# Performance work log

Measured on AMD Instinct MI355X. Metric: run time of the kernel, lower is better.

The kernel has to match this reference:

```python
import jax, jax.numpy as jnp
import numpy as np

B, N, KNB, F, H = 1, 50000, 16, 128, 128
BN_EPS = 1e-3  # keras BatchNormalization default epsilon
ALPHA = 0.3    # keras LeakyReLU default negative slope


def setup_inputs() -> dict:
    key = jax.random.key(0)
    ks = jax.random.split(key, 14)
    s_in = 1.0 / np.sqrt(F)
    s_cat = 1.0 / np.sqrt(F + H)
    return {
        'embeddings': jax.random.normal(ks[0], (B, N, F), jnp.float32),
        'weights': jnp.zeros((1, 1), jnp.float32),  # unused in call_att
        'neighbor_set': jax.random.randint(ks[1], (B, N, KNB), 0, N),
        'Wq': jax.random.normal(ks[2], (F, H), jnp.float32) * s_in,
        'bq': jnp.zeros((H,), jnp.float32),
        'Wk': jax.random.normal(ks[3], (F, H), jnp.float32) * s_in,
        'bk': jnp.zeros((H,), jnp.float32),
        'Wv': jax.random.normal(ks[4], (F, H), jnp.float32) * s_in,
        'bv': jnp.zeros((H,), jnp.float32),
        'W1': jax.random.normal(ks[5], (F + H, H), jnp.float32) * s_cat,
        'b1': jnp.zeros((H,), jnp.float32),
        'gamma': 1.0 + 0.1 * jax.random.normal(ks[6], (H,), jnp.float32),
        'beta': 0.1 * jax.random.normal(ks[7], (H,), jnp.float32),
        'mov_mean': 0.1 * jax.random.normal(ks[8], (H,), jnp.float32),
        'mov_var': 1.0 + 0.1 * jax.random.uniform(ks[9], (H,), jnp.float32),
    }


def reference(embeddings, weights, neighbor_set, Wq, bq, Wk, bk, Wv, bv,
              W1, b1, gamma, beta, mov_mean, mov_var):
    lrelu = lambda x: jax.nn.leaky_relu(x, ALPHA)
    # batched gather: nb[b, n, k] = embeddings[b, neighbor_set[b, n, k]]  -> [B,N,K,F]
    nb = jax.vmap(lambda e, idx: e[idx])(embeddings, neighbor_set)
    q = lrelu(embeddings @ Wq + bq)      # [B,N,H]
    k = lrelu(nb @ Wk + bk)              # [B,N,K,H]
    v = lrelu(nb @ Wv + bv)              # [B,N,K,H]
    # Q is tiled across the K neighbor rows in the original; every attention row
    # is identical, so mean-pool over rows == single-query attention. Same math.
    scores = jnp.einsum('bnh,bnkh->bnk', q, k)          # dot-product, no scale
    attn = jax.nn.softmax(scores, axis=-1)
    pooled = jnp.einsum('bnk,bnkh->bnh', attn, v)       # [B,N,H]
    h = lrelu(jnp.concatenate([embeddings, pooled], axis=-1) @ W1 + b1)
    h = h / (jnp.linalg.norm(h, axis=2, keepdims=True) + 1e-6)
    # BatchNormalization (inference form, axis=-1)
    return gamma * (h - mov_mean) * jax.lax.rsqrt(mov_var + BN_EPS) + beta
```

## Files before the change

### kernel.cpp

```cpp
#include <hip/hip_runtime.h>
#include <hip/hip_bf16.h>

#define N_NODES 50000
#define KNB 16
#define FDIM 128
#define HDIM 128
#define ALPHA 0.3f
#define BN_EPS 1e-3f

typedef __bf16 v8bf __attribute__((ext_vector_type(8)));
typedef float v4f __attribute__((ext_vector_type(4)));
typedef unsigned short ushort_t;

__device__ __forceinline__ float blo(unsigned int u) {
    union { float f; unsigned int i; } x; x.i = u << 16; return x.f;
}
__device__ __forceinline__ float bhi(unsigned int u) {
    union { float f; unsigned int i; } x; x.i = u & 0xffff0000u; return x.f;
}

__device__ __forceinline__ unsigned short f2bf(float f) {
    union { float f; unsigned int u; } x;
    x.f = f;
    unsigned int r = x.u + 0x7fffu + ((x.u >> 16) & 1u);
    return (unsigned short)(r >> 16);
}

__device__ __forceinline__ unsigned int pk2(float a, float b) {
    __hip_bfloat162 h = __float22bfloat162_rn(make_float2(a, b));
    union { __hip_bfloat162 h; unsigned int u; } r; r.h = h; return r.u;
}

__device__ __forceinline__ float lrelu(float x) { return x > 0.f ? x : ALPHA * x; }

__device__ __forceinline__ v8bf load8f(const float* p) {
    float4 A = ((const float4*)p)[0];
    float4 B = ((const float4*)p)[1];
    union { v8bf v; unsigned int u[4]; } r;
    r.u[0] = pk2(A.x, A.y); r.u[1] = pk2(A.z, A.w);
    r.u[2] = pk2(B.x, B.y); r.u[3] = pk2(B.z, B.w);
    return r.v;
}

__global__ __launch_bounds__(256) void prep_kernel(
    const float* __restrict__ Wq, const float* __restrict__ Wk,
    const float* __restrict__ Wv, const float* __restrict__ W1,
    ushort_t* __restrict__ WT)
{
    const int idx = blockIdx.x * 256 + threadIdx.x;
    if (idx < 16384) {
        int k = idx >> 7, n = idx & 127;
        WT[n * 128 + k] = f2bf(Wq[idx]);
    } else if (idx < 32768) {
        int i = idx - 16384; int k = i >> 7, n = i & 127;
        WT[16384 + n * 128 + k] = f2bf(Wk[i]);
    } else if (idx < 49152) {
        int i = idx - 32768; int k = i >> 7, n = i & 127;
        WT[32768 + n * 128 + k] = f2bf(Wv[i]);
    } else if (idx < 81920) {
        int i = idx - 49152; int k = i >> 7, n = i & 127;
        WT[49152 + n * 256 + k] = f2bf(W1[i]);
    }
}

__global__ __launch_bounds__(256) void qkv_kernel(
    const float* __restrict__ E, const ushort_t* __restrict__ WT,
    const float* __restrict__ bq, const float* __restrict__ bk,
    const float* __restrict__ bv,
    float* __restrict__ Qo, ushort_t* __restrict__ KV)
{
    __shared__ ushort_t sW[128 * 136];

    const int tid  = threadIdx.x;
    const int wave = tid >> 6;
    const int lane = tid & 63;
    const int quad = lane >> 4;
    const int j    = lane & 15;
    const int row0 = blockIdx.x * 128 + wave * 32;

    const int ar0 = min(row0 + j,      N_NODES - 1);
    const int ar1 = min(row0 + 16 + j, N_NODES - 1);

    v8bf a0f[4], a1f[4];
#pragma unroll
    for (int ks = 0; ks < 4; ++ks) {
        const int k0 = ks * 32 + quad * 8;
        a0f[ks] = load8f(E + (size_t)ar0 * FDIM + k0);
        a1f[ks] = load8f(E + (size_t)ar1 * FDIM + k0);
    }

    const float* biases[3] = {bq, bk, bv};

    for (int w = 0; w < 3; ++w) {
        const ushort_t* Wsrc = WT + w * 16384;
        for (int i = tid; i < 2048; i += 256) {
            int n = i >> 4, kc = i & 15;
            *(uint4*)(&sW[n * 136 + kc * 8]) = *(const uint4*)(Wsrc + n * 128 + kc * 8);
        }
        __syncthreads();

        v4f acc[2][8];
#pragma unroll
        for (int rb = 0; rb < 2; ++rb)
#pragma unroll
            for (int c = 0; c < 8; ++c) acc[rb][c] = (v4f){0.f, 0.f, 0.f, 0.f};

#pragma unroll
        for (int ks = 0; ks < 4; ++ks) {
            const int k0 = ks * 32 + quad * 8;
            v8bf b[8];
#pragma unroll
            for (int c = 0; c < 8; ++c)
                b[c] = *(const v8bf*)(&sW[(c * 16 + j) * 136 + k0]);
#pragma unroll
            for (int c = 0; c < 8; ++c) {
                acc[0][c] = __builtin_amdgcn_mfma_f32_16x16x32_bf16(a0f[ks], b[c], acc[0][c], 0, 0, 0);
                acc[1][c] = __builtin_amdgcn_mfma_f32_16x16x32_bf16(a1f[ks], b[c], acc[1][c], 0, 0, 0);
            }
        }

        const float* bias = biases[w];
#pragma unroll
        for (int c = 0; c < 8; ++c) {
            const int col = c * 16 + j;
            const float bv_ = bias[col];
#pragma unroll
            for (int rb = 0; rb < 2; ++rb) {
#pragma unroll
                for (int i = 0; i < 4; ++i) {
                    const int r = row0 + rb * 16 + quad * 4 + i;
                    if (r < N_NODES) {
                        const float x = lrelu(acc[rb][c][i] + bv_);
                        if (w == 0)      Qo[(size_t)r * HDIM + col] = x;
                        else if (w == 1) KV[(size_t)r * 256 + col] = f2bf(x);
                        else             KV[(size_t)r * 256 + 128 + col] = f2bf(x);
                    }
                }
            }
        }
        __syncthreads();
    }
}

__global__ __launch_bounds__(256) void attn_kernel(
    float* __restrict__ QP, const ushort_t* __restrict__ KV,
    const int* __restrict__ nbr)
{
    const int tid  = threadIdx.x;
    const int wave = tid >> 6;
    const int lane = tid & 63;
    const int node = __builtin_amdgcn_readfirstlane(blockIdx.x * 4 + wave);

    const float2 qp = ((const float2*)(QP + (size_t)node * HDIM))[lane];

    int idxs[KNB];
    const int* nb = nbr + node * KNB;
#pragma unroll
    for (int t = 0; t < KNB; ++t) {
        int id = nb[t];
        idxs[t] = ((unsigned)id < (unsigned)N_NODES) ? id : 0;
    }

    float sc[KNB];
#pragma unroll
    for (int t = 0; t < KNB; ++t) {
        const unsigned int kp = ((const unsigned int*)(KV + (size_t)idxs[t] * 256))[lane];
        float p = qp.x * blo(kp) + qp.y * bhi(kp);
#pragma unroll
        for (int off = 32; off >= 1; off >>= 1) p += __shfl_xor(p, off, 64);
        sc[t] = p;
    }

    float m = sc[0];
#pragma unroll
    for (int t = 1; t < KNB; ++t) m = fmaxf(m, sc[t]);
    float s = 0.f;
#pragma unroll
    for (int t = 0; t < KNB; ++t) { sc[t] = __expf(sc[t] - m); s += sc[t]; }
    const float inv = 1.f / s;

    float p0 = 0.f, p1 = 0.f;
#pragma unroll
    for (int t = 0; t < KNB; ++t) {
        const unsigned int vp = ((const unsigned int*)(KV + (size_t)idxs[t] * 256 + 128))[lane];
        const float a = sc[t] * inv;
        p0 += a * blo(vp);
        p1 += a * bhi(vp);
    }

    ((float2*)(QP + (size_t)node * HDIM))[lane] = make_float2(p0, p1);
}

__global__ __launch_bounds__(256) void out_kernel(
    const float* __restrict__ E, const ushort_t* __restrict__ W1T,
    const float* __restrict__ b1,
    const float* __restrict__ gamma, const float* __restrict__ beta,
    const float* __restrict__ mmean, const float* __restrict__ mvar,
    float* __restrict__ OutP)
{
    __shared__ ushort_t sW[128 * 136];

    const int tid  = threadIdx.x;
    const int wave = tid >> 6;
    const int lane = tid & 63;
    const int quad = lane >> 4;
    const int j    = lane & 15;
    const int row0 = blockIdx.x * 128 + wave * 32;

    const int ar0 = min(row0 + j,      N_NODES - 1);
    const int ar1 = min(row0 + 16 + j, N_NODES - 1);

    v4f acc[2][8];
#pragma unroll
    for (int rb = 0; rb < 2; ++rb)
#pragma unroll
        for (int c = 0; c < 8; ++c) acc[rb][c] = (v4f){0.f, 0.f, 0.f, 0.f};

    for (int half = 0; half < 2; ++half) {
        for (int i = tid; i < 2048; i += 256) {
            int n = i >> 4, kc = i & 15;
            *(uint4*)(&sW[n * 136 + kc * 8]) =
                *(const uint4*)(W1T + n * 256 + half * 128 + kc * 8);
        }
        __syncthreads();

        const float* Abase = (half == 0) ? E : (const float*)OutP;
#pragma unroll
        for (int ks = 0; ks < 4; ++ks) {
            const int k0 = ks * 32 + quad * 8;
            v8bf a0 = load8f(Abase + (size_t)ar0 * 128 + k0);
            v8bf a1 = load8f(Abase + (size_t)ar1 * 128 + k0);
            v8bf b[8];
#pragma unroll
            for (int c = 0; c < 8; ++c)
                b[c] = *(const v8bf*)(&sW[(c * 16 + j) * 136 + k0]);
#pragma unroll
            for (int c = 0; c < 8; ++c) {
                acc[0][c] = __builtin_amdgcn_mfma_f32_16x16x32_bf16(a0, b[c], acc[0][c], 0, 0, 0);
                acc[1][c] = __builtin_amdgcn_mfma_f32_16x16x32_bf16(a1, b[c], acc[1][c], 0, 0, 0);
            }
        }
        __syncthreads();
    }

    float scale_[8], shift_[8], bias_[8];
#pragma unroll
    for (int c = 0; c < 8; ++c) {
        const int col = c * 16 + j;
        const float sc = gamma[col] * rsqrtf(mvar[col] + BN_EPS);
        scale_[c] = sc;
        shift_[c] = beta[col] - mmean[col] * sc;
        bias_[c]  = b1[col];
    }

#pragma unroll
    for (int rb = 0; rb < 2; ++rb)
#pragma unroll
        for (int c = 0; c < 8; ++c)
#pragma unroll
            for (int i = 0; i < 4; ++i)
                acc[rb][c][i] = lrelu(acc[rb][c][i] + bias_[c]);

#pragma unroll
    for (int rb = 0; rb < 2; ++rb) {
#pragma unroll
        for (int i = 0; i < 4; ++i) {
            float ss = 0.f;
#pragma unroll
            for (int c = 0; c < 8; ++c) ss += acc[rb][c][i] * acc[rb][c][i];
            ss += __shfl_xor(ss, 1, 64);
            ss += __shfl_xor(ss, 2, 64);
            ss += __shfl_xor(ss, 4, 64);
            ss += __shfl_xor(ss, 8, 64);
            const float invn = 1.f / (sqrtf(ss) + 1e-6f);
            const int r = row0 + rb * 16 + quad * 4 + i;
            if (r < N_NODES) {
#pragma unroll
                for (int c = 0; c < 8; ++c)
                    OutP[(size_t)r * HDIM + c * 16 + j] =
                        acc[rb][c][i] * invn * scale_[c] + shift_[c];
            }
        }
    }
}

extern "C" void kernel_launch(void* const* d_in, const int* in_sizes, int n_in,
                              void* d_out, int out_size, void* d_ws, size_t ws_size,
                              hipStream_t stream)
{
    const float* E     = (const float*)d_in[0];
    const int*   nbr   = (const int*)d_in[2];
    const float* Wq    = (const float*)d_in[3];
    const float* bq    = (const float*)d_in[4];
    const float* Wk    = (const float*)d_in[5];
    const float* bk    = (const float*)d_in[6];
    const float* Wv    = (const float*)d_in[7];
    const float* bv    = (const float*)d_in[8];
    const float* W1    = (const float*)d_in[9];
    const float* b1    = (const float*)d_in[10];
    const float* gam   = (const float*)d_in[11];
    const float* bet   = (const float*)d_in[12];
    const float* mmean = (const float*)d_in[13];
    const float* mvar  = (const float*)d_in[14];

    ushort_t* KV = (ushort_t*)d_ws;
    ushort_t* WT = KV + (size_t)N_NODES * 256;
    float* QP = (float*)d_out;

    const int gridA = (N_NODES + 127) / 128;
    prep_kernel<<<320, 256, 0, stream>>>(Wq, Wk, Wv, W1, WT);
    qkv_kernel<<<gridA, 256, 0, stream>>>(E, WT, bq, bk, bv, QP, KV);
    attn_kernel<<<N_NODES / 4, 256, 0, stream>>>(QP, KV, nbr);
    out_kernel<<<gridA, 256, 0, stream>>>(E, WT + 49152, b1, gam, bet, mmean, mvar, QP);
}
```

Measured before the change: 218.3 us.

## Split QKV projection across grid y and read weights directly from global

The QKV kernel now launches a 2D grid with one y-slice per projection (Q, K, V) instead of looping over the three weight matrices inside each block. Both the QKV and output kernels drop the shared-memory weight staging and its barriers, loading MFMA B fragments straight from global memory and relying on cache. This gives three times as many blocks and frees LDS for occupancy. The cost is that each embedding row is loaded three times and B-fragment loads become uncoalesced cached global reads instead of LDS reads.

```diff
diff --git a/kernel.cpp b/kernel.cpp
--- a/kernel.cpp
+++ b/kernel.cpp
@@ -69,14 +69,15 @@
     const float* __restrict__ bv,
     float* __restrict__ Qo, ushort_t* __restrict__ KV)
 {
-    __shared__ ushort_t sW[128 * 136];
-
     const int tid  = threadIdx.x;
     const int wave = tid >> 6;
     const int lane = tid & 63;
     const int quad = lane >> 4;
     const int j    = lane & 15;
     const int row0 = blockIdx.x * 128 + wave * 32;
+    const int w    = blockIdx.y;
+
+    const ushort_t* __restrict__ Wsrc = WT + w * 16384;
 
     const int ar0 = min(row0 + j,      N_NODES - 1);
     const int ar1 = min(row0 + 16 + j, N_NODES - 1);
@@ -89,56 +90,44 @@
         a1f[ks] = load8f(E + (size_t)ar1 * FDIM + k0);
     }
 
-    const float* biases[3] = {bq, bk, bv};
-
-    for (int w = 0; w < 3; ++w) {
-        const ushort_t* Wsrc = WT + w * 16384;
-        for (int i = tid; i < 2048; i += 256) {
-            int n = i >> 4, kc = i & 15;
-            *(uint4*)(&sW[n * 136 + kc * 8]) = *(const uint4*)(Wsrc + n * 128 + kc * 8);
-        }
-        __syncthreads();
-
-        v4f acc[2][8];
-#pragma unroll
-        for (int rb = 0; rb < 2; ++rb)
-#pragma unroll
-            for (int c = 0; c < 8; ++c) acc[rb][c] = (v4f){0.f, 0.f, 0.f, 0.f};
-
-#pragma unroll
-        for (int ks = 0; ks < 4; ++ks) {
-            const int k0 = ks * 32 + quad * 8;
-            v8bf b[8];
-#pragma unroll
-            for (int c = 0; c < 8; ++c)
-                b[c] = *(const v8bf*)(&sW[(c * 16 + j) * 136 + k0]);
-#pragma unroll
-            for (int c = 0; c < 8; ++c) {
-                acc[0][c] = __builtin_amdgcn_mfma_f32_16x16x32_bf16(a0f[ks], b[c], acc[0][c], 0, 0, 0);
-                acc[1][c] = __builtin_amdgcn_mfma_f32_16x16x32_bf16(a1f[ks], b[c], acc[1][c], 0, 0, 0);
-            }
-        }
-
-        const float* bias = biases[w];
+    v4f acc[2][8];
+#pragma unroll
+    for (int rb = 0; rb < 2; ++rb)
+#pragma unroll
+        for (int c = 0; c < 8; ++c) acc[rb][c] = (v4f){0.f, 0.f, 0.f, 0.f};
+
+#pragma unroll
+    for (int ks = 0; ks < 4; ++ks) {
+        const int k0 = ks * 32 + quad * 8;
+        v8bf b[8];
+#pragma unroll
+        for (int c = 0; c < 8; ++c)
+            b[c] = *(const v8bf*)(Wsrc + (c * 16 + j) * 128 + k0);
 #pragma unroll
         for (int c = 0; c < 8; ++c) {
-            const int col = c * 16 + j;
-            const float bv_ = bias[col];
-#pragma unroll
-            for (int rb = 0; rb < 2; ++rb) {
-#pragma unroll
-                for (int i = 0; i < 4; ++i) {
-                    const int r = row0 + rb * 16 + quad * 4 + i;
-                    if (r < N_NODES) {
-                        const float x = lrelu(acc[rb][c][i] + bv_);
-                        if (w == 0)      Qo[(size_t)r * HDIM + col] = x;
-                        else if (w == 1) KV[(size_t)r * 256 + col] = f2bf(x);
-                        else             KV[(size_t)r * 256 + 128 + col] = f2bf(x);
-                    }
+            acc[0][c] = __builtin_amdgcn_mfma_f32_16x16x32_bf16(a0f[ks], b[c], acc[0][c], 0, 0, 0);
+            acc[1][c] = __builtin_amdgcn_mfma_f32_16x16x32_bf16(a1f[ks], b[c], acc[1][c], 0, 0, 0);
+        }
+    }
+
+    const float* __restrict__ bias = (w == 0) ? bq : (w == 1) ? bk : bv;
+#pragma unroll
+    for (int c = 0; c < 8; ++c) {
+        const int col = c * 16 + j;
+        const float bv_ = bias[col];
+#pragma unroll
+        for (int rb = 0; rb < 2; ++rb) {
+#pragma unroll
+            for (int i = 0; i < 4; ++i) {
+                const int r = row0 + rb * 16 + quad * 4 + i;
+                if (r < N_NODES) {
+                    const float x = lrelu(acc[rb][c][i] + bv_);
+                    if (w == 0)      Qo[(size_t)r * HDIM + col] = x;
+                    else if (w == 1) KV[(size_t)r * 256 + col] = f2bf(x);
+                    else             KV[(size_t)r * 256 + 128 + col] = f2bf(x);
                 }
             }
         }
-        __syncthreads();
     }
 }
 
@@ -198,8 +187,6 @@
     const float* __restrict__ mmean, const float* __restrict__ mvar,
     float* __restrict__ OutP)
 {
-    __shared__ ushort_t sW[128 * 136];
-
     const int tid  = threadIdx.x;
     const int wave = tid >> 6;
     const int lane = tid & 63;
@@ -216,15 +203,10 @@
 #pragma unroll
         for (int c = 0; c < 8; ++c) acc[rb][c] = (v4f){0.f, 0.f, 0.f, 0.f};
 
+#pragma unroll
     for (int half = 0; half < 2; ++half) {
-        for (int i = tid; i < 2048; i += 256) {
-            int n = i >> 4, kc = i & 15;
-            *(uint4*)(&sW[n * 136 + kc * 8]) =
-                *(const uint4*)(W1T + n * 256 + half * 128 + kc * 8);
-        }
-        __syncthreads();
-
-        const float* Abase = (half == 0) ? E : (const float*)OutP;
+        const float* __restrict__ Abase = (half == 0) ? E : (const float*)OutP;
+        const ushort_t* __restrict__ Wh = W1T + half * 128;
 #pragma unroll
         for (int ks = 0; ks < 4; ++ks) {
             const int k0 = ks * 32 + quad * 8;
@@ -233,15 +215,16 @@
             v8bf b[8];
 #pragma unroll
             for (int c = 0; c < 8; ++c)
-                b[c] = *(const v8bf*)(&sW[(c * 16 + j) * 136 + k0]);
+                b[c] = *(const v8bf*)(Wh + (c * 16 + j) * 256 + k0);
 #pragma unroll
             for (int c = 0; c < 8; ++c) {
                 acc[0][c] = __builtin_amdgcn_mfma_f32_16x16x32_bf16(a0, b[c], acc[0][c], 0, 0, 0);
                 acc[1][c] = __builtin_amdgcn_mfma_f32_16x16x32_bf16(a1, b[c], acc[1][c], 0, 0, 0);
             }
         }
-        __syncthreads();
-    }
+    }
+
+    __syncthreads();
 
     float scale_[8], shift_[8], bias_[8];
 #pragma unroll
@@ -309,7 +292,7 @@
 
     const int gridA = (N_NODES + 127) / 128;
     prep_kernel<<<320, 256, 0, stream>>>(Wq, Wk, Wv, W1, WT);
-    qkv_kernel<<<gridA, 256, 0, stream>>>(E, WT, bq, bk, bv, QP, KV);
+    qkv_kernel<<<dim3(gridA, 3), 256, 0, stream>>>(E, WT, bq, bk, bv, QP, KV);
     attn_kernel<<<N_NODES / 4, 256, 0, stream>>>(QP, KV, nbr);
     out_kernel<<<gridA, 256, 0, stream>>>(E, WT + 49152, b1, gam, bet, mmean, mvar, QP);
 }
```

Result: slower. 236.0 us (+8.1%).

## Stage QKV outputs through per-wave LDS for coalesced stores; read weights from global

Applied to the files above, without the earlier changes.

Removes the shared-memory weight staging and block-wide barriers in the QKV projection, so each wave reads the transposed bf16 weights directly from global memory (cached in L1/L2). The MFMA operands are swapped so each lane holds four consecutive output columns, which are biased, activated and written into a per-wave LDS tile. Rows are then written back with 16-byte coalesced stores instead of scattered 4-byte and 2-byte stores. The trade-off is more global/L2 traffic for weight loads, and it relies on a pk2 helper being defined elsewhere in the file.

```diff
diff --git a/kernel.cpp b/kernel.cpp
--- a/kernel.cpp
+++ b/kernel.cpp
@@ -63,13 +63,17 @@
     }
 }
 
+#define QSTRIDE 560
+#define KVSTRIDE 528
+#define WTILE 18432
+
 __global__ __launch_bounds__(256) void qkv_kernel(
     const float* __restrict__ E, const ushort_t* __restrict__ WT,
     const float* __restrict__ bq, const float* __restrict__ bk,
     const float* __restrict__ bv,
     float* __restrict__ Qo, ushort_t* __restrict__ KV)
 {
-    __shared__ ushort_t sW[128 * 136];
+    __shared__ char smem[4 * WTILE];
 
     const int tid  = threadIdx.x;
     const int wave = tid >> 6;
@@ -78,6 +82,8 @@
     const int j    = lane & 15;
     const int row0 = blockIdx.x * 128 + wave * 32;
 
+    char* const wbase = smem + wave * WTILE;
+
     const int ar0 = min(row0 + j,      N_NODES - 1);
     const int ar1 = min(row0 + 16 + j, N_NODES - 1);
 
@@ -92,12 +98,7 @@
     const float* biases[3] = {bq, bk, bv};
 
     for (int w = 0; w < 3; ++w) {
-        const ushort_t* Wsrc = WT + w * 16384;
-        for (int i = tid; i < 2048; i += 256) {
-            int n = i >> 4, kc = i & 15;
-            *(uint4*)(&sW[n * 136 + kc * 8]) = *(const uint4*)(Wsrc + n * 128 + kc * 8);
-        }
-        __syncthreads();
+        const ushort_t* __restrict__ Wsrc = WT + w * 16384;
 
         v4f acc[2][8];
 #pragma unroll
@@ -111,34 +112,59 @@
             v8bf b[8];
 #pragma unroll
             for (int c = 0; c < 8; ++c)
-                b[c] = *(const v8bf*)(&sW[(c * 16 + j) * 136 + k0]);
+                b[c] = *(const v8bf*)(Wsrc + (c * 16 + j) * 128 + k0);
 #pragma unroll
             for (int c = 0; c < 8; ++c) {
-                acc[0][c] = __builtin_amdgcn_mfma_f32_16x16x32_bf16(a0f[ks], b[c], acc[0][c], 0, 0, 0);
-                acc[1][c] = __builtin_amdgcn_mfma_f32_16x16x32_bf16(a1f[ks], b[c], acc[1][c], 0, 0, 0);
-            }
-        }
-
-        const float* bias = biases[w];
-#pragma unroll
-        for (int c = 0; c < 8; ++c) {
-            const int col = c * 16 + j;
-            const float bv_ = bias[col];
-#pragma unroll
-            for (int rb = 0; rb < 2; ++rb) {
-#pragma unroll
-                for (int i = 0; i < 4; ++i) {
-                    const int r = row0 + rb * 16 + quad * 4 + i;
-                    if (r < N_NODES) {
-                        const float x = lrelu(acc[rb][c][i] + bv_);
-                        if (w == 0)      Qo[(size_t)r * HDIM + col] = x;
-                        else if (w == 1) KV[(size_t)r * 256 + col] = f2bf(x);
-                        else             KV[(size_t)r * 256 + 128 + col] = f2bf(x);
-                    }
+                acc[0][c] = __builtin_amdgcn_mfma_f32_16x16x32_bf16(b[c], a0f[ks], acc[0][c], 0, 0, 0);
+                acc[1][c] = __builtin_amdgcn_mfma_f32_16x16x32_bf16(b[c], a1f[ks], acc[1][c], 0, 0, 0);
+            }
+        }
+
+        const float* __restrict__ bias = biases[w];
+
+        if (w == 0) {
+#pragma unroll
+            for (int rb = 0; rb < 2; ++rb)
+#pragma unroll
+                for (int c = 0; c < 8; ++c) {
+                    const float4 bb = ((const float4*)bias)[c * 4 + quad];
+                    v4f v = acc[rb][c];
+                    v[0] = lrelu(v[0] + bb.x); v[1] = lrelu(v[1] + bb.y);
+                    v[2] = lrelu(v[2] + bb.z); v[3] = lrelu(v[3] + bb.w);
+                    *(v4f*)(wbase + (rb * 16 + j) * QSTRIDE + (c * 16 + quad * 4) * 4) = v;
                 }
-            }
-        }
-        __syncthreads();
+#pragma unroll
+            for (int t = 0; t < 16; ++t) {
+                const int r  = 2 * t + (lane >> 5);
+                const v4f v  = *(const v4f*)(wbase + r * QSTRIDE + (lane & 31) * 16);
+                const int gr = row0 + r;
+                if (gr < N_NODES)
+                    *(v4f*)(Qo + (size_t)gr * HDIM + (lane & 31) * 4) = v;
+            }
+        } else {
+            const int voff = (w == 2) ? 256 : 0;
+#pragma unroll
+            for (int rb = 0; rb < 2; ++rb)
+#pragma unroll
+                for (int c = 0; c < 8; ++c) {
+                    const float4 bb = ((const float4*)bias)[c * 4 + quad];
+                    const v4f v = acc[rb][c];
+                    uint2 u;
+                    u.x = pk2(lrelu(v[0] + bb.x), lrelu(v[1] + bb.y));
+                    u.y = pk2(lrelu(v[2] + bb.z), lrelu(v[3] + bb.w));
+                    *(uint2*)(wbase + (rb * 16 + j) * KVSTRIDE + (c * 16 + quad * 4) * 2 + voff) = u;
+                }
+            if (w == 2) {
+#pragma unroll
+                for (int t = 0; t < 16; ++t) {
+                    const int r  = 2 * t + (lane >> 5);
+                    const uint4 v = *(const uint4*)(wbase + r * KVSTRIDE + (lane & 31) * 16);
+                    const int gr = row0 + r;
+                    if (gr < N_NODES)
+                        *(uint4*)((char*)KV + (size_t)gr * 512 + (lane & 31) * 16) = v;
+                }
+            }
+        }
     }
 }
 
```

After: 209.8 us (median of 2 runs). 1.04x faster.
